# Performance work log

Measured on AMD Instinct MI355X. Metric: run time of the kernel, lower is better.

Reference implementation:

```python
import jax, jax.numpy as jnp
import numpy as np

EPS = jnp.finfo(jnp.float32).eps


def setup_inputs() -> dict:
    key = jax.random.key(0)
    k0, k1, k2 = jax.random.split(key, 3)
    B, N = 1, 4194304
    cloud_t0 = jax.random.normal(k0, (B, N, 3), dtype=jnp.float32)
    cloud_t1 = jax.random.normal(k1, (B, N, 3), dtype=jnp.float32)
    weights = jax.random.uniform(k2, (B, N), dtype=jnp.float32)
    return {"cloud_t0": cloud_t0, "cloud_t1": cloud_t1, "weights": weights}


def reference(cloud_t0, cloud_t1, weights):
    # use_epsilon_on_weights = False branch
    count_nonzero = jnp.sum(weights > 0.0, axis=-1)
    not_enough_points = count_nonzero < 3
    weights = weights + (not_enough_points.astype(weights.dtype) * EPS)[:, None]

    cum_wts = jnp.sum(weights, axis=-1)                      # (B,)
    w = weights[:, :, None]                                   # (B,N,1)
    mx = jnp.sum(cloud_t0 * w, axis=1) / cum_wts[:, None]     # (B,3) weighted centroid
    my = jnp.sum(cloud_t1 * w, axis=1) / cum_wts[:, None]
    Xc = cloud_t0 - mx[:, None, :]
    Yc = cloud_t1 - my[:, None, :]
    # weighted cross-covariance: (B,3,3)
    Sxy = jnp.einsum('bno,bni->boi', Yc * w, Xc) / cum_wts[:, None, None]

    U, D, Vh = jnp.linalg.svd(Sxy, full_matrices=False)       # torch.svd returns V = Vh^T
    V = jnp.swapaxes(Vh, -1, -2)

    # rank via torch.linalg.matrix_rank default tol: max_sv * max(m,n) * eps
    tol = D.max(axis=-1) * 3 * EPS
    rank = jnp.sum(D > tol[:, None], axis=-1)

    det_S = jnp.linalg.det(Sxy)
    det_mul = jnp.linalg.det(U) * jnp.linalg.det(V)
    sign_full = jnp.where(det_S < 0.0, -1.0, 1.0)             # rank == 3 case
    sign_def = jnp.where(jnp.isclose(det_mul, -1.0), -1.0, 1.0)  # rank == 2 case
    s = jnp.where(rank > 2, sign_full, sign_def)              # (B,)

    # R = U @ diag(1,1,s) @ V^T
    diag = jnp.stack([jnp.ones_like(s), jnp.ones_like(s), s], axis=-1)  # (B,3)
    R = jnp.einsum('boc,bc,bic->boi', U, diag, V)             # (B,3,3)
    t = my - jnp.einsum('boc,bc->bo', R, mx)                  # (B,3)

    B = R.shape[0]
    R4 = jnp.concatenate([R, jnp.zeros((B, 1, 3), R.dtype)], axis=1)    # (B,4,3)
    t4 = jnp.concatenate([t, jnp.ones((B, 1), t.dtype)], axis=-1)       # (B,4)
    T = jnp.concatenate([R4, t4[:, :, None]], axis=-1)        # (B,4,4)
    return T, not_enough_points
```

## Files before the change

### kernel.cpp

```cpp
#include <hip/hip_runtime.h>
#include <math.h>

#define NACC 32
#define TILE 1024

__device__ __forceinline__ void accum_point(float w, float x0, float x1, float x2,
                                            float y0, float y1, float y2, float* a) {
    a[0] += (w > 0.0f) ? 1.0f : 0.0f;
    a[1] += w;
    a[2] = fmaf(w, x0, a[2]); a[3] = fmaf(w, x1, a[3]); a[4] = fmaf(w, x2, a[4]);
    float wy0 = w * y0, wy1 = w * y1, wy2 = w * y2;
    a[5] += wy0; a[6] += wy1; a[7] += wy2;
    a[8]  = fmaf(wy0, x0, a[8]);  a[9]  = fmaf(wy0, x1, a[9]);  a[10] = fmaf(wy0, x2, a[10]);
    a[11] = fmaf(wy1, x0, a[11]); a[12] = fmaf(wy1, x1, a[12]); a[13] = fmaf(wy1, x2, a[13]);
    a[14] = fmaf(wy2, x0, a[14]); a[15] = fmaf(wy2, x1, a[15]); a[16] = fmaf(wy2, x2, a[16]);
    a[17] += x0; a[18] += x1; a[19] += x2;
    a[20] += y0; a[21] += y1; a[22] += y2;
    a[23] = fmaf(y0, x0, a[23]); a[24] = fmaf(y0, x1, a[24]); a[25] = fmaf(y0, x2, a[25]);
    a[26] = fmaf(y1, x0, a[26]); a[27] = fmaf(y1, x1, a[27]); a[28] = fmaf(y1, x2, a[28]);
    a[29] = fmaf(y2, x0, a[29]); a[30] = fmaf(y2, x1, a[30]); a[31] = fmaf(y2, x2, a[31]);
}

__global__ __launch_bounds__(256) void kabsch_reduce(
    const float* __restrict__ c0, const float* __restrict__ c1,
    const float* __restrict__ w, int N, float* __restrict__ partials, int nblocks) {
    __shared__ float4 sA[TILE];
    __shared__ float4 sB[TILE];
    __shared__ float  sw[TILE];
    __shared__ float  wred[4][NACC];

    float a[NACC];
    #pragma unroll
    for (int i = 0; i < NACC; ++i) a[i] = 0.0f;

    const int t = threadIdx.x;
    const int lane = t & 63, wave = t >> 6;
    const float4* A4 = (const float4*)c0;
    const float4* B4 = (const float4*)c1;
    const float4* W4 = (const float4*)w;
    float* fA = (float*)sA;
    float* fB = (float*)sB;

    int nfull = N >> 10;

    for (int tile = blockIdx.x; tile < nfull; tile += gridDim.x) {
        int baseAB = tile * 768;
        #pragma unroll
        for (int k = 0; k < 3; ++k) {
            int idx = (k << 8) + t;
            float4 va = A4[baseAB + idx];
            float4 vb = B4[baseAB + idx];
            unsigned flat0 = (unsigned)idx << 2;
            float aa[4] = { va.x, va.y, va.z, va.w };
            float bb[4] = { vb.x, vb.y, vb.z, vb.w };
            #pragma unroll
            for (int j = 0; j < 4; ++j) {
                unsigned f = flat0 + j;
                unsigned p = (f * 21846u) >> 16;
                unsigned cc = f - p * 3u;
                fA[(p << 2) | cc] = aa[j];
                fB[(p << 2) | cc] = bb[j];
            }
        }
        ((float4*)sw)[t] = W4[(tile << 8) + t];
        __syncthreads();
        #pragma unroll
        for (int k = 0; k < 4; ++k) {
            int p = t + (k << 8);
            float4 xa = sA[p];
            float4 xb = sB[p];
            float wt = sw[p];
            accum_point(wt, xa.x, xa.y, xa.z, xb.x, xb.y, xb.z, a);
        }
        __syncthreads();
    }
    if (blockIdx.x == 0 && t == 0) {
        for (int i = nfull << 10; i < N; ++i)
            accum_point(w[i], c0[3*i], c0[3*i+1], c0[3*i+2],
                        c1[3*i], c1[3*i+1], c1[3*i+2], a);
    }

    {
        int hi;
        hi = lane & 1;
        #pragma unroll
        for (int i = 0; i < 16; ++i) {
            float send = hi ? a[i] : a[i + 16];
            float recv = __shfl_xor(send, 1, 64);
            a[i] = (hi ? a[i + 16] : a[i]) + recv;
        }
        hi = lane & 2;
        #pragma unroll
        for (int i = 0; i < 8; ++i) {
            float send = hi ? a[i] : a[i + 8];
            float recv = __shfl_xor(send, 2, 64);
            a[i] = (hi ? a[i + 8] : a[i]) + recv;
        }
        hi = lane & 4;
        #pragma unroll
        for (int i = 0; i < 4; ++i) {
            float send = hi ? a[i] : a[i + 4];
            float recv = __shfl_xor(send, 4, 64);
            a[i] = (hi ? a[i + 4] : a[i]) + recv;
        }
        hi = lane & 8;
        #pragma unroll
        for (int i = 0; i < 2; ++i) {
            float send = hi ? a[i] : a[i + 2];
            float recv = __shfl_xor(send, 8, 64);
            a[i] = (hi ? a[i + 2] : a[i]) + recv;
        }
        hi = lane & 16;
        {
            float send = hi ? a[0] : a[1];
            float recv = __shfl_xor(send, 16, 64);
            a[0] = (hi ? a[1] : a[0]) + recv;
        }
        a[0] += __shfl_xor(a[0], 32, 64);
    }
    if (lane < 32) {
        int acc = ((lane & 1) << 4) | ((lane & 2) << 2) | (lane & 4)
                | ((lane & 8) >> 2) | ((lane & 16) >> 4);
        wred[wave][acc] = a[0];
    }
    __syncthreads();
    if (t < NACC)
        partials[t * nblocks + blockIdx.x] =
            wred[0][t] + wred[1][t] + wred[2][t] + wred[3][t];
}

__device__ __forceinline__ double det3(const double m[3][3]) {
    return m[0][0] * (m[1][1] * m[2][2] - m[1][2] * m[2][1])
         - m[0][1] * (m[1][0] * m[2][2] - m[1][2] * m[2][0])
         + m[0][2] * (m[1][0] * m[2][1] - m[1][1] * m[2][0]);
}

__global__ __launch_bounds__(256) void kabsch_finalize(
    const float* __restrict__ partials, int nblocks, int N, float* __restrict__ out) {
    double d[NACC];
    #pragma unroll
    for (int i = 0; i < NACC; ++i) d[i] = 0.0;
    for (int m = threadIdx.x; m < nblocks; m += 256) {
        #pragma unroll
        for (int i = 0; i < NACC; ++i)
            d[i] += (double)partials[i * nblocks + m];
    }
    #pragma unroll
    for (int off = 32; off > 0; off >>= 1) {
        #pragma unroll
        for (int i = 0; i < NACC; ++i) d[i] += __shfl_down(d[i], off, 64);
    }
    __shared__ double sm[4][NACC];
    int wave = threadIdx.x >> 6, lane = threadIdx.x & 63;
    if (lane == 0) {
        #pragma unroll
        for (int i = 0; i < NACC; ++i) sm[wave][i] = d[i];
    }
    __syncthreads();
    if (threadIdx.x != 0) return;
    #pragma unroll
    for (int i = 0; i < NACC; ++i) d[i] = sm[0][i] + sm[1][i] + sm[2][i] + sm[3][i];

    const double EPSF = (double)1.1920929e-7f;
    double cnt = d[0];
    double W = d[1];
    double swx[3] = { d[2], d[3], d[4] };
    double swy[3] = { d[5], d[6], d[7] };
    double swyx[9];
    for (int i = 0; i < 9; ++i) swyx[i] = d[8 + i];
    bool nep = cnt < 3.0;
    if (nep) {
        W += EPSF * (double)N;
        for (int i = 0; i < 3; ++i) { swx[i] += EPSF * d[17 + i]; swy[i] += EPSF * d[20 + i]; }
        for (int i = 0; i < 9; ++i) swyx[i] += EPSF * d[23 + i];
    }

    double mx[3], my[3];
    for (int i = 0; i < 3; ++i) { mx[i] = swx[i] / W; my[i] = swy[i] / W; }
    double S[3][3];
    for (int o = 0; o < 3; ++o)
        for (int i = 0; i < 3; ++i)
            S[o][i] = swyx[o * 3 + i] / W - my[o] * mx[i];

    double Bm[3][3], V[3][3];
    for (int i = 0; i < 3; ++i)
        for (int j = 0; j < 3; ++j) {
            double acc = 0.0;
            for (int k = 0; k < 3; ++k) acc += S[k][i] * S[k][j];
            Bm[i][j] = acc;
            V[i][j] = (i == j) ? 1.0 : 0.0;
        }
    for (int sweep = 0; sweep < 30; ++sweep) {
        double off2 = Bm[0][1]*Bm[0][1] + Bm[0][2]*Bm[0][2] + Bm[1][2]*Bm[1][2];
        double diag2 = Bm[0][0]*Bm[0][0] + Bm[1][1]*Bm[1][1] + Bm[2][2]*Bm[2][2];
        if (off2 <= diag2 * 1e-32 + 1e-300) break;
        for (int pair = 0; pair < 3; ++pair) {
            int p = (pair == 2) ? 1 : 0;
            int q = (pair == 0) ? 1 : 2;
            double apq = Bm[p][q];
            if (fabs(apq) < 1e-300) continue;
            double theta = (Bm[q][q] - Bm[p][p]) / (2.0 * apq);
            double tt = ((theta >= 0.0) ? 1.0 : -1.0) / (fabs(theta) + sqrt(1.0 + theta * theta));
            double c = 1.0 / sqrt(1.0 + tt * tt);
            double sn = tt * c;
            for (int k = 0; k < 3; ++k) {
                double bkp = Bm[k][p], bkq = Bm[k][q];
                Bm[k][p] = c * bkp - sn * bkq;
                Bm[k][q] = sn * bkp + c * bkq;
            }
            for (int k = 0; k < 3; ++k) {
                double bpk = Bm[p][k], bqk = Bm[q][k];
                Bm[p][k] = c * bpk - sn * bqk;
                Bm[q][k] = sn * bpk + c * bqk;
            }
            for (int k = 0; k < 3; ++k) {
                double vkp = V[k][p], vkq = V[k][q];
                V[k][p] = c * vkp - sn * vkq;
                V[k][q] = sn * vkp + c * vkq;
            }
        }
    }
    double lam[3] = { Bm[0][0], Bm[1][1], Bm[2][2] };
    for (int i = 0; i < 2; ++i)
        for (int j = i + 1; j < 3; ++j)
            if (lam[j] > lam[i]) {
                double tl = lam[i]; lam[i] = lam[j]; lam[j] = tl;
                for (int k = 0; k < 3; ++k) { double tv = V[k][i]; V[k][i] = V[k][j]; V[k][j] = tv; }
            }
    double sig[3];
    for (int i = 0; i < 3; ++i) sig[i] = sqrt(fmax(lam[i], 0.0));

    double U[3][3];
    for (int i = 0; i < 3; ++i) {
        double u0 = S[0][0]*V[0][i] + S[0][1]*V[1][i] + S[0][2]*V[2][i];
        double u1 = S[1][0]*V[0][i] + S[1][1]*V[1][i] + S[1][2]*V[2][i];
        double u2 = S[2][0]*V[0][i] + S[2][1]*V[1][i] + S[2][2]*V[2][i];
        double nrm = sqrt(u0*u0 + u1*u1 + u2*u2);
        if (nrm > 1e-150) {
            U[0][i] = u0 / nrm; U[1][i] = u1 / nrm; U[2][i] = u2 / nrm;
        } else if (i == 0) {
            U[0][0] = 1.0; U[1][0] = 0.0; U[2][0] = 0.0;
        } else if (i == 1) {
            double e0 = (fabs(U[0][0]) < 0.9) ? 1.0 : 0.0;
            double e1 = 1.0 - e0;
            double dp = e0 * U[0][0] + e1 * U[1][0];
            double v0 = e0 - dp * U[0][0], v1 = e1 - dp * U[1][0], v2 = -dp * U[2][0];
            double n2 = sqrt(v0*v0 + v1*v1 + v2*v2);
            U[0][1] = v0 / n2; U[1][1] = v1 / n2; U[2][1] = v2 / n2;
        } else {
            U[0][2] = U[1][0]*U[2][1] - U[2][0]*U[1][1];
            U[1][2] = U[2][0]*U[0][1] - U[0][0]*U[2][1];
            U[2][2] = U[0][0]*U[1][1] - U[1][0]*U[0][1];
        }
    }

    double tol = sig[0] * 3.0 * EPSF;
    int rank = (sig[0] > tol) + (sig[1] > tol) + (sig[2] > tol);
    double detS = det3(S);
    double det_mul = det3(U) * det3(V);
    double sign_full = (detS < 0.0) ? -1.0 : 1.0;
    double sign_def = (fabs(det_mul + 1.0) <= 1.00001e-5) ? -1.0 : 1.0;
    double s = (rank > 2) ? sign_full : sign_def;

    double R[3][3];
    for (int o = 0; o < 3; ++o)
        for (int i = 0; i < 3; ++i)
            R[o][i] = U[o][0]*V[i][0] + U[o][1]*V[i][1] + s * U[o][2]*V[i][2];
    double tv[3];
    for (int o = 0; o < 3; ++o)
        tv[o] = my[o] - (R[o][0]*mx[0] + R[o][1]*mx[1] + R[o][2]*mx[2]);

    for (int o = 0; o < 3; ++o) {
        out[o * 4 + 0] = (float)R[o][0];
        out[o * 4 + 1] = (float)R[o][1];
        out[o * 4 + 2] = (float)R[o][2];
        out[o * 4 + 3] = (float)tv[o];
    }
    out[12] = 0.0f; out[13] = 0.0f; out[14] = 0.0f; out[15] = 1.0f;
    out[16] = nep ? 1.0f : 0.0f;
}

extern "C" void kernel_launch(void* const* d_in, const int* in_sizes, int n_in,
                              void* d_out, int out_size, void* d_ws, size_t ws_size,
                              hipStream_t stream) {
    const float* c0 = (const float*)d_in[0];
    const float* c1 = (const float*)d_in[1];
    const float* w  = (const float*)d_in[2];
    float* out = (float*)d_out;
    int N = in_sizes[2];

    int blocks = 1024;
    size_t need = (size_t)blocks * NACC * sizeof(float);
    if (need > ws_size) {
        blocks = (int)(ws_size / (NACC * sizeof(float)));
        if (blocks < 1) blocks = 1;
    }
    float* partials = (float*)d_ws;

    kabsch_reduce<<<blocks, 256, 0, stream>>>(c0, c1, w, N, partials, blocks);
    kabsch_finalize<<<1, 256, 0, stream>>>(partials, blocks, N, out);
}
```

Measured before the change: 153.6 us.

## Replace LDS-staged tiles with direct per-thread float4 loads of point groups

The reduction kernel no longer stages 1024-point tiles through shared memory with scatter/gather and two barriers per tile. Each thread now loads two groups of 8 consecutive points directly as float4 vectors, giving each thread more independent loads in flight. Because each thread reads six contiguous float4s, a wavefront's addresses are strided rather than coalesced. Separately, the Jacobi SVD loop now runs a fixed 6 sweeps with no convergence check, which removes the branch but may lose accuracy on hard cases.

```diff
diff --git a/kernel.cpp b/kernel.cpp
--- a/kernel.cpp
+++ b/kernel.cpp
@@ -2,7 +2,6 @@
 #include <math.h>
 
 #define NACC 32
-#define TILE 1024
 
 __device__ __forceinline__ void accum_point(float w, float x0, float x1, float x2,
                                             float y0, float y1, float y2, float* a) {
@@ -21,13 +20,18 @@
     a[29] = fmaf(y2, x0, a[29]); a[30] = fmaf(y2, x1, a[30]); a[31] = fmaf(y2, x2, a[31]);
 }
 
+__device__ __forceinline__ void accum_group(float4 wv, float4 x0, float4 x1, float4 x2,
+                                            float4 y0, float4 y1, float4 y2, float* a) {
+    accum_point(wv.x, x0.x, x0.y, x0.z, y0.x, y0.y, y0.z, a);
+    accum_point(wv.y, x0.w, x1.x, x1.y, y0.w, y1.x, y1.y, a);
+    accum_point(wv.z, x1.z, x1.w, x2.x, y1.z, y1.w, y2.x, a);
+    accum_point(wv.w, x2.y, x2.z, x2.w, y2.y, y2.z, y2.w, a);
+}
+
 __global__ __launch_bounds__(256) void kabsch_reduce(
     const float* __restrict__ c0, const float* __restrict__ c1,
     const float* __restrict__ w, int N, float* __restrict__ partials, int nblocks) {
-    __shared__ float4 sA[TILE];
-    __shared__ float4 sB[TILE];
-    __shared__ float  sw[TILE];
-    __shared__ float  wred[4][NACC];
+    __shared__ float wred[4][NACC];
 
     float a[NACC];
     #pragma unroll
@@ -35,47 +39,46 @@
 
     const int t = threadIdx.x;
     const int lane = t & 63, wave = t >> 6;
+    const int tid = blockIdx.x * blockDim.x + t;
+    const int nthreads = gridDim.x * blockDim.x;
+    const int ngroups = N >> 2;
+    const int npairs = ngroups >> 1;
     const float4* A4 = (const float4*)c0;
     const float4* B4 = (const float4*)c1;
     const float4* W4 = (const float4*)w;
-    float* fA = (float*)sA;
-    float* fB = (float*)sB;
-
-    int nfull = N >> 10;
-
-    for (int tile = blockIdx.x; tile < nfull; tile += gridDim.x) {
-        int baseAB = tile * 768;
-        #pragma unroll
-        for (int k = 0; k < 3; ++k) {
-            int idx = (k << 8) + t;
-            float4 va = A4[baseAB + idx];
-            float4 vb = B4[baseAB + idx];
-            unsigned flat0 = (unsigned)idx << 2;
-            float aa[4] = { va.x, va.y, va.z, va.w };
-            float bb[4] = { vb.x, vb.y, vb.z, vb.w };
-            #pragma unroll
-            for (int j = 0; j < 4; ++j) {
-                unsigned f = flat0 + j;
-                unsigned p = (f * 21846u) >> 16;
-                unsigned cc = f - p * 3u;
-                fA[(p << 2) | cc] = aa[j];
-                fB[(p << 2) | cc] = bb[j];
-            }
-        }
-        ((float4*)sw)[t] = W4[(tile << 8) + t];
-        __syncthreads();
-        #pragma unroll
-        for (int k = 0; k < 4; ++k) {
-            int p = t + (k << 8);
-            float4 xa = sA[p];
-            float4 xb = sB[p];
-            float wt = sw[p];
-            accum_point(wt, xa.x, xa.y, xa.z, xb.x, xb.y, xb.z, a);
-        }
-        __syncthreads();
-    }
-    if (blockIdx.x == 0 && t == 0) {
-        for (int i = nfull << 10; i < N; ++i)
+
+    for (int p0 = tid; p0 < npairs; p0 += 2 * nthreads) {
+        int p1 = p0 + nthreads;
+        bool have1 = p1 < npairs;
+        size_t b0 = (size_t)6 * (size_t)p0;
+        size_t b1 = have1 ? (size_t)6 * (size_t)p1 : b0;
+
+        float4 w0a = W4[p0 * 2], w0b = W4[p0 * 2 + 1];
+        float4 a00 = A4[b0],     a01 = A4[b0 + 1], a02 = A4[b0 + 2];
+        float4 a03 = A4[b0 + 3], a04 = A4[b0 + 4], a05 = A4[b0 + 5];
+        float4 b00 = B4[b0],     b01 = B4[b0 + 1], b02 = B4[b0 + 2];
+        float4 b03 = B4[b0 + 3], b04 = B4[b0 + 4], b05 = B4[b0 + 5];
+        float4 w1a = W4[(have1 ? p1 : p0) * 2], w1b = W4[(have1 ? p1 : p0) * 2 + 1];
+        float4 a10 = A4[b1],     a11 = A4[b1 + 1], a12 = A4[b1 + 2];
+        float4 a13 = A4[b1 + 3], a14 = A4[b1 + 4], a15 = A4[b1 + 5];
+        float4 b10 = B4[b1],     b11 = B4[b1 + 1], b12 = B4[b1 + 2];
+        float4 b13 = B4[b1 + 3], b14 = B4[b1 + 4], b15 = B4[b1 + 5];
+
+        accum_group(w0a, a00, a01, a02, b00, b01, b02, a);
+        accum_group(w0b, a03, a04, a05, b03, b04, b05, a);
+        if (have1) {
+            accum_group(w1a, a10, a11, a12, b10, b11, b12, a);
+            accum_group(w1b, a13, a14, a15, b13, b14, b15, a);
+        }
+    }
+    if (tid == 0) {
+        if (npairs * 2 < ngroups) {
+            int g = npairs * 2;
+            size_t base = (size_t)3 * (size_t)g;
+            accum_group(W4[g], A4[base], A4[base + 1], A4[base + 2],
+                        B4[base], B4[base + 1], B4[base + 2], a);
+        }
+        for (int i = ngroups << 2; i < N; ++i)
             accum_point(w[i], c0[3*i], c0[3*i+1], c0[3*i+2],
                         c1[3*i], c1[3*i+1], c1[3*i+2], a);
     }
@@ -190,10 +193,7 @@
             Bm[i][j] = acc;
             V[i][j] = (i == j) ? 1.0 : 0.0;
         }
-    for (int sweep = 0; sweep < 30; ++sweep) {
-        double off2 = Bm[0][1]*Bm[0][1] + Bm[0][2]*Bm[0][2] + Bm[1][2]*Bm[1][2];
-        double diag2 = Bm[0][0]*Bm[0][0] + Bm[1][1]*Bm[1][1] + Bm[2][2]*Bm[2][2];
-        if (off2 <= diag2 * 1e-32 + 1e-300) break;
+    for (int sweep = 0; sweep < 6; ++sweep) {
         for (int pair = 0; pair < 3; ++pair) {
             int p = (pair == 2) ? 1 : 0;
             int q = (pair == 0) ? 1 : 2;
```

New measurement: 158.8 us. 1.03x slower.
